# Optimization experiments

Hardware: AMD Instinct MI355X
Metric: run time of the kernel (lower is better)

## Reference

```python
import jax, jax.numpy as jnp
import numpy as np

B, T, I, H = 64, 512, 512, 512


def setup_inputs() -> dict:
    key = jax.random.key(0)
    ks = jax.random.split(key, 7)
    xavier_std = float(np.sqrt(2.0 / (B + H)))  # matches xavier_normal_ on [B,H]
    w_scale = float(1.0 / np.sqrt(H))           # ~ pytorch LSTMCell default scale
    return {
        "x": jax.random.normal(ks[0], (B, T, I), dtype=jnp.float32),
        "h0": jax.random.normal(ks[1], (B, H), dtype=jnp.float32) * xavier_std,
        "c0": jax.random.normal(ks[2], (B, H), dtype=jnp.float32) * xavier_std,
        "W_ih": jax.random.normal(ks[3], (4 * H, I), dtype=jnp.float32) * w_scale,
        "W_hh": jax.random.normal(ks[4], (4 * H, H), dtype=jnp.float32) * w_scale,
        "b_ih": jax.random.normal(ks[5], (4 * H,), dtype=jnp.float32) * w_scale,
        "b_hh": jax.random.normal(ks[6], (4 * H,), dtype=jnp.float32) * w_scale,
    }


def lstm_forward(x, h0, c0, W_ih, W_hh, b_ih, b_hh):
    # Precompute the input-to-gate projection for all timesteps in one big GEMM.
    # xg: [T, B, 4H]
    xg = jnp.einsum("bti,gi->tbg", x, W_ih) + (b_ih + b_hh)

    def step(carry, xg_t):
        h, c = carry
        gates = xg_t + h @ W_hh.T  # [B, 4H]
        i, f, g, o = jnp.split(gates, 4, axis=-1)
        i = jax.nn.sigmoid(i)
        f = jax.nn.sigmoid(f)
        g = jnp.tanh(g)
        o = jax.nn.sigmoid(o)
        c = f * c + i * g
        h = o * jnp.tanh(c)
        return (h, c), h

    (h_T, c_T), outs = jax.lax.scan(step, (h0, c0), xg)
    output = jnp.transpose(outs, (1, 0, 2))  # [B, T, H]
    return output, h_T, c_T


def reference(x, h0, c0, W_ih, W_hh, b_ih, b_hh):
    return lstm_forward(x, h0, c0, W_ih, W_hh, b_ih, b_hh)
```

## Files before the change

kernel.cpp:

```cpp
#include <hip/hip_runtime.h>
#include <hip/hip_fp16.h>
#include <string.h>

constexpr int B = 64, T = 512, I = 512, H = 512, G = 2048;

typedef _Float16 half8 __attribute__((ext_vector_type(8)));
typedef float floatx4 __attribute__((ext_vector_type(4)));

__global__ __launch_bounds__(256, 2) void xg_gemm(
    const float* __restrict__ x,
    const float* __restrict__ W_ih,
    const float* __restrict__ b_ih,
    const float* __restrict__ b_hh,
    _Float16* __restrict__ xg)
{
    const int tid  = threadIdx.x;
    const int wave = tid >> 6, lane = tid & 63;
    const int quad = lane >> 4, col = lane & 15;
    const int rowA = blockIdx.x * 128 + wave * 16;
    const int rowB = rowA + 64;

    __shared__ __align__(16) _Float16 xs[64][264];

    half8 wfA[16], wfB[16];
    {
        const float* wpA = W_ih + (size_t)(rowA + col) * I;
        const float* wpB = W_ih + (size_t)(rowB + col) * I;
#pragma unroll
        for (int kc = 0; kc < 16; ++kc) {
            half8 vA, vB;
#pragma unroll
            for (int j = 0; j < 8; ++j) {
                vA[j] = (_Float16)wpA[kc * 32 + quad * 8 + j];
                vB[j] = (_Float16)wpB[kc * 32 + quad * 8 + j];
            }
            wfA[kc] = vA; wfB[kc] = vB;
        }
    }
    float biasA[4], biasB[4];
#pragma unroll
    for (int r = 0; r < 4; ++r) {
        biasA[r] = b_ih[rowA + quad * 4 + r] + b_hh[rowA + quad * 4 + r];
        biasB[r] = b_ih[rowB + quad * 4 + r] + b_hh[rowB + quad * 4 + r];
    }

    for (int ti = 0; ti < 4; ++ti) {
        const int t = blockIdx.y * 4 + ti;
        floatx4 accA[4], accB[4];
#pragma unroll
        for (int nt = 0; nt < 4; ++nt) {
            accA[nt] = (floatx4){0.f, 0.f, 0.f, 0.f};
            accB[nt] = (floatx4){0.f, 0.f, 0.f, 0.f};
        }

        for (int hfl = 0; hfl < 2; ++hfl) {
            __syncthreads();
#pragma unroll 4
            for (int c = 0; c < 16; ++c) {
                int idx = c * 256 + tid;
                int row = idx >> 6;
                int kk  = (idx & 63) * 4;
                const float4 v = *(const float4*)(x + ((size_t)row * T + t) * I + hfl * 256 + kk);
                xs[row][kk + 0] = (_Float16)v.x;
                xs[row][kk + 1] = (_Float16)v.y;
                xs[row][kk + 2] = (_Float16)v.z;
                xs[row][kk + 3] = (_Float16)v.w;
            }
            __syncthreads();
#pragma unroll
            for (int kc = 0; kc < 8; ++kc) {
#pragma unroll
                for (int nt = 0; nt < 4; ++nt) {
                    const half8 bfr = *(const half8*)&xs[nt * 16 + col][kc * 32 + quad * 8];
                    accA[nt] = __builtin_amdgcn_mfma_f32_16x16x32_f16(
                        wfA[hfl * 8 + kc], bfr, accA[nt], 0, 0, 0);
                    accB[nt] = __builtin_amdgcn_mfma_f32_16x16x32_f16(
                        wfB[hfl * 8 + kc], bfr, accB[nt], 0, 0, 0);
                }
            }
        }
#pragma unroll
        for (int nt = 0; nt < 4; ++nt) {
            int b = nt * 16 + col;
#pragma unroll
            for (int r = 0; r < 4; ++r) {
                xg[((size_t)t * G + rowA + quad * 4 + r) * B + b] = (_Float16)(accA[nt][r] + biasA[r]);
                xg[((size_t)t * G + rowB + quad * 4 + r) * B + b] = (_Float16)(accB[nt][r] + biasB[r]);
            }
        }
    }
}

__global__ __launch_bounds__(256, 1) void lstm_rec(
    const float* __restrict__ h0,
    const float* __restrict__ c0,
    const float* __restrict__ W_hh,
    const _Float16* __restrict__ xg,
    _Float16* __restrict__ hbuf,
    unsigned int* __restrict__ cnts,
    float* __restrict__ out)
{
    const int blk  = blockIdx.x;
    const int bg   = blk & 3;
    const int hg   = blk >> 2;
    const int tid  = threadIdx.x;
    const int wave = tid >> 6, lane = tid & 63;
    const int quad = lane >> 4, col = lane & 15;

    const int bglob = bg * 16 + col;
    const int hbase = hg * 32 + wave * 8;

    unsigned int* cnt = cnts + bg * 64;

    int arow0 = (col < 8) ? (hbase + col) : (512 + hbase + col - 8);
    int arow1 = arow0 + 1024;
    half8 wf0[16], wf1[16];
#pragma unroll
    for (int kc = 0; kc < 16; ++kc) {
        const float* p0 = W_hh + (size_t)arow0 * H + kc * 32 + quad * 8;
        const float* p1 = W_hh + (size_t)arow1 * H + kc * 32 + quad * 8;
        half8 v0, v1;
#pragma unroll
        for (int j = 0; j < 8; ++j) { v0[j] = (_Float16)p0[j]; v1[j] = (_Float16)p1[j]; }
        wf0[kc] = v0; wf1[kc] = v1;
    }

    int xrow0[4], xrow1[4];
#pragma unroll
    for (int r = 0; r < 4; ++r) {
        int lr = quad * 4 + r;
        xrow0[r] = (lr < 8) ? (hbase + lr) : (512 + hbase + lr - 8);
        xrow1[r] = xrow0[r] + 1024;
    }

    float c[4];
#pragma unroll
    for (int r = 0; r < 4; ++r)
        c[r] = c0[(size_t)bglob * H + hbase + (quad & 1) * 4 + r];

    _Float16* hb0 = hbuf + ((size_t)0 * 4 + bg) * 16 * 512;
    _Float16* hb1 = hbuf + ((size_t)1 * 4 + bg) * 16 * 512;

    if (quad < 2) {
        _Float16 v4[4];
#pragma unroll
        for (int r = 0; r < 4; ++r)
            v4[r] = (_Float16)h0[(size_t)bglob * H + hbase + (quad & 1) * 4 + r];
        unsigned long long uv; __builtin_memcpy(&uv, v4, 8);
        __hip_atomic_store((unsigned long long*)(hb0 + (size_t)col * 512 + hbase + (quad & 1) * 4),
                           uv, __ATOMIC_RELAXED, __HIP_MEMORY_SCOPE_AGENT);
    }
    asm volatile("s_waitcnt vmcnt(0)" ::: "memory");
    __syncthreads();
    if (tid == 0)
        __hip_atomic_fetch_add(cnt, 1u, __ATOMIC_RELAXED, __HIP_MEMORY_SCOPE_AGENT);

    float xp0[4], xp1[4];
#pragma unroll
    for (int r = 0; r < 4; ++r) {
        xp0[r] = (float)xg[(size_t)xrow0[r] * B + bglob];
        xp1[r] = (float)xg[(size_t)xrow1[r] * B + bglob];
    }

    while (__hip_atomic_load(cnt, __ATOMIC_RELAXED, __HIP_MEMORY_SCOPE_AGENT) < 16u) {}
    asm volatile("" ::: "memory");

    float hh[4] = {0.f, 0.f, 0.f, 0.f};

    for (int t = 0; t < T; ++t) {
        const _Float16* hcur = (t & 1) ? hb1 : hb0;
        _Float16*       hnxt = (t & 1) ? hb0 : hb1;

        unsigned long long hu0[16], hu1[16];
#pragma unroll
        for (int kc = 0; kc < 16; ++kc) {
            unsigned long long* hp =
                (unsigned long long*)(hcur + (size_t)col * 512 + kc * 32 + quad * 8);
            hu0[kc] = __hip_atomic_load(hp,     __ATOMIC_RELAXED, __HIP_MEMORY_SCOPE_AGENT);
            hu1[kc] = __hip_atomic_load(hp + 1, __ATOMIC_RELAXED, __HIP_MEMORY_SCOPE_AGENT);
        }

        floatx4 acc0 = (floatx4){0.f, 0.f, 0.f, 0.f};
        floatx4 acc1 = (floatx4){0.f, 0.f, 0.f, 0.f};
#pragma unroll
        for (int kc = 0; kc < 16; ++kc) {
            half8 bfr;
            __builtin_memcpy(&bfr, &hu0[kc], 8);
            __builtin_memcpy((char*)&bfr + 8, &hu1[kc], 8);
            acc0 = __builtin_amdgcn_mfma_f32_16x16x32_f16(wf0[kc], bfr, acc0, 0, 0, 0);
            acc1 = __builtin_amdgcn_mfma_f32_16x16x32_f16(wf1[kc], bfr, acc1, 0, 0, 0);
        }

        float p0[4], p1[4];
#pragma unroll
        for (int r = 0; r < 4; ++r) {
            p0[r] = acc0[r] + xp0[r];
            p1[r] = acc1[r] + xp1[r];
        }
        float e0[4], e1[4];
#pragma unroll
        for (int r = 0; r < 4; ++r) {
            e0[r] = __shfl_xor(p0[r], 32);
            e1[r] = __shfl_xor(p1[r], 32);
        }
#pragma unroll
        for (int r = 0; r < 4; ++r) {
            float iv = (quad < 2) ? p0[r] : e0[r];
            float fv = (quad < 2) ? e0[r] : p0[r];
            float gv = (quad < 2) ? p1[r] : e1[r];
            float ov = (quad < 2) ? e1[r] : p1[r];
            float ii = 1.f / (1.f + __expf(-iv));
            float ff = 1.f / (1.f + __expf(-fv));
            float eg = __expf(-2.f * gv);
            float gg = (1.f - eg) / (1.f + eg);
            float oo = 1.f / (1.f + __expf(-ov));
            float cn = ff * c[r] + ii * gg;
            c[r] = cn;
            float ec = __expf(-2.f * cn);
            hh[r] = oo * ((1.f - ec) / (1.f + ec));
        }
        if (quad < 2) {
            _Float16 v4[4] = {(_Float16)hh[0], (_Float16)hh[1],
                              (_Float16)hh[2], (_Float16)hh[3]};
            unsigned long long uv; __builtin_memcpy(&uv, v4, 8);
            __hip_atomic_store((unsigned long long*)(hnxt + (size_t)col * 512 + hbase + (quad & 1) * 4),
                               uv, __ATOMIC_RELAXED, __HIP_MEMORY_SCOPE_AGENT);
            float* op = out + ((size_t)bglob * T + t) * H + hbase + (quad & 1) * 4;
            op[0] = hh[0]; op[1] = hh[1]; op[2] = hh[2]; op[3] = hh[3];
        }

        asm volatile("s_waitcnt vmcnt(0)" ::: "memory");
        __syncthreads();
        if (tid == 0)
            __hip_atomic_fetch_add(cnt, 1u, __ATOMIC_RELAXED, __HIP_MEMORY_SCOPE_AGENT);

        if (t + 1 < T) {
            const _Float16* xgt = xg + (size_t)(t + 1) * G * B;
#pragma unroll
            for (int r = 0; r < 4; ++r) {
                xp0[r] = (float)xgt[(size_t)xrow0[r] * B + bglob];
                xp1[r] = (float)xgt[(size_t)xrow1[r] * B + bglob];
            }
            const unsigned int tgt = 16u * (unsigned)(t + 2);
            while (__hip_atomic_load(cnt, __ATOMIC_RELAXED, __HIP_MEMORY_SCOPE_AGENT) < tgt) {}
            asm volatile("" ::: "memory");
        }
    }

    if (quad < 2) {
        float* hT = out + (size_t)B * T * H;
        float* cT = hT + (size_t)B * H;
#pragma unroll
        for (int r = 0; r < 4; ++r) {
            int jj = (quad & 1) * 4 + r;
            hT[(size_t)bglob * H + hbase + jj] = hh[r];
            cT[(size_t)bglob * H + hbase + jj] = c[r];
        }
    }
}

extern "C" void kernel_launch(void* const* d_in, const int* in_sizes, int n_in,
                              void* d_out, int out_size, void* d_ws, size_t ws_size,
                              hipStream_t stream) {
    const float* x    = (const float*)d_in[0];
    const float* h0   = (const float*)d_in[1];
    const float* c0   = (const float*)d_in[2];
    const float* W_ih = (const float*)d_in[3];
    const float* W_hh = (const float*)d_in[4];
    const float* b_ih = (const float*)d_in[5];
    const float* b_hh = (const float*)d_in[6];
    float* out = (float*)d_out;

    unsigned int* cnts = (unsigned int*)d_ws;
    _Float16* hbuf = (_Float16*)((char*)d_ws + 2048);
    _Float16* xg   = (_Float16*)((char*)d_ws + 2048 + (size_t)2 * 4 * 16 * 512 * 2);

    hipMemsetAsync(d_ws, 0, 2048, stream);

    xg_gemm<<<dim3(16, 128), 256, 0, stream>>>(x, W_ih, b_ih, b_hh, xg);
    lstm_rec<<<64, 256, 0, stream>>>(h0, c0, W_hh, xg, hbuf, cnts, out);
}
```

Measured before the change: 3.112 ms.

## Replace block-wide atomic counter barrier with per-wave flags polled by whole wave

The cross-block step barrier changes from a __syncthreads plus a single atomic fetch_add counter to one flag per wave (64 flags per batch group). Each wave stores its own timestep flag, and every wave polls all 64 flags in parallel with one load per lane and __all. The next-step xg prefetch is moved before the MFMA loop so its latency overlaps compute, and the output store is moved after the flag publish. This removes the intra-block barrier and atomic RMW contention, at the cost of more polling traffic and a dependence on relaxed-ordering assumptions.

```diff
diff --git a/kernel.cpp b/kernel.cpp
--- a/kernel.cpp
+++ b/kernel.cpp
@@ -97,7 +97,7 @@
     const float* __restrict__ W_hh,
     const _Float16* __restrict__ xg,
     _Float16* __restrict__ hbuf,
-    unsigned int* __restrict__ cnts,
+    unsigned int* __restrict__ flags,
     float* __restrict__ out)
 {
     const int blk  = blockIdx.x;
@@ -110,7 +110,8 @@
     const int bglob = bg * 16 + col;
     const int hbase = hg * 32 + wave * 8;
 
-    unsigned int* cnt = cnts + bg * 64;
+    unsigned int* flg   = flags + bg * 64;
+    unsigned int* myflg = flg + hg * 4 + wave;
 
     int arow0 = (col < 8) ? (hbase + col) : (512 + hbase + col - 8);
     int arow1 = arow0 + 1024;
@@ -151,9 +152,8 @@
                            uv, __ATOMIC_RELAXED, __HIP_MEMORY_SCOPE_AGENT);
     }
     asm volatile("s_waitcnt vmcnt(0)" ::: "memory");
-    __syncthreads();
-    if (tid == 0)
-        __hip_atomic_fetch_add(cnt, 1u, __ATOMIC_RELAXED, __HIP_MEMORY_SCOPE_AGENT);
+    if (lane == 0)
+        __hip_atomic_store(myflg, 1u, __ATOMIC_RELAXED, __HIP_MEMORY_SCOPE_AGENT);
 
     float xp0[4], xp1[4];
 #pragma unroll
@@ -162,7 +162,10 @@
         xp1[r] = (float)xg[(size_t)xrow1[r] * B + bglob];
     }
 
-    while (__hip_atomic_load(cnt, __ATOMIC_RELAXED, __HIP_MEMORY_SCOPE_AGENT) < 16u) {}
+    for (;;) {
+        unsigned f = __hip_atomic_load(flg + lane, __ATOMIC_RELAXED, __HIP_MEMORY_SCOPE_AGENT);
+        if (__all(f >= 1u)) break;
+    }
     asm volatile("" ::: "memory");
 
     float hh[4] = {0.f, 0.f, 0.f, 0.f};
@@ -178,6 +181,17 @@
                 (unsigned long long*)(hcur + (size_t)col * 512 + kc * 32 + quad * 8);
             hu0[kc] = __hip_atomic_load(hp,     __ATOMIC_RELAXED, __HIP_MEMORY_SCOPE_AGENT);
             hu1[kc] = __hip_atomic_load(hp + 1, __ATOMIC_RELAXED, __HIP_MEMORY_SCOPE_AGENT);
+        }
+        asm volatile("" ::: "memory");
+
+        float xn0[4], xn1[4];
+        if (t + 1 < T) {
+            const _Float16* xgt = xg + (size_t)(t + 1) * G * B;
+#pragma unroll
+            for (int r = 0; r < 4; ++r) {
+                xn0[r] = (float)xgt[(size_t)xrow0[r] * B + bglob];
+                xn1[r] = (float)xgt[(size_t)xrow1[r] * B + bglob];
+            }
         }
 
         floatx4 acc0 = (floatx4){0.f, 0.f, 0.f, 0.f};
@@ -225,24 +239,25 @@
             unsigned long long uv; __builtin_memcpy(&uv, v4, 8);
             __hip_atomic_store((unsigned long long*)(hnxt + (size_t)col * 512 + hbase + (quad & 1) * 4),
                                uv, __ATOMIC_RELAXED, __HIP_MEMORY_SCOPE_AGENT);
+        }
+
+        asm volatile("s_waitcnt vmcnt(0)" ::: "memory");
+        if (lane == 0)
+            __hip_atomic_store(myflg, (unsigned)(t + 2), __ATOMIC_RELAXED, __HIP_MEMORY_SCOPE_AGENT);
+
+        if (quad < 2) {
             float* op = out + ((size_t)bglob * T + t) * H + hbase + (quad & 1) * 4;
             op[0] = hh[0]; op[1] = hh[1]; op[2] = hh[2]; op[3] = hh[3];
         }
 
-        asm volatile("s_waitcnt vmcnt(0)" ::: "memory");
-        __syncthreads();
-        if (tid == 0)
-            __hip_atomic_fetch_add(cnt, 1u, __ATOMIC_RELAXED, __HIP_MEMORY_SCOPE_AGENT);
-
         if (t + 1 < T) {
-            const _Float16* xgt = xg + (size_t)(t + 1) * G * B;
-#pragma unroll
-            for (int r = 0; r < 4; ++r) {
-                xp0[r] = (float)xgt[(size_t)xrow0[r] * B + bglob];
-                xp1[r] = (float)xgt[(size_t)xrow1[r] * B + bglob];
-            }
-            const unsigned int tgt = 16u * (unsigned)(t + 2);
-            while (__hip_atomic_load(cnt, __ATOMIC_RELAXED, __HIP_MEMORY_SCOPE_AGENT) < tgt) {}
+#pragma unroll
+            for (int r = 0; r < 4; ++r) { xp0[r] = xn0[r]; xp1[r] = xn1[r]; }
+            const unsigned tgt = (unsigned)(t + 2);
+            for (;;) {
+                unsigned f = __hip_atomic_load(flg + lane, __ATOMIC_RELAXED, __HIP_MEMORY_SCOPE_AGENT);
+                if (__all(f >= tgt)) break;
+            }
             asm volatile("" ::: "memory");
         }
     }
@@ -271,12 +286,12 @@
     const float* b_hh = (const float*)d_in[6];
     float* out = (float*)d_out;
 
-    unsigned int* cnts = (unsigned int*)d_ws;
+    unsigned int* flags = (unsigned int*)d_ws;
     _Float16* hbuf = (_Float16*)((char*)d_ws + 2048);
     _Float16* xg   = (_Float16*)((char*)d_ws + 2048 + (size_t)2 * 4 * 16 * 512 * 2);
 
     hipMemsetAsync(d_ws, 0, 2048, stream);
 
     xg_gemm<<<dim3(16, 128), 256, 0, stream>>>(x, W_ih, b_ih, b_hh, xg);
-    lstm_rec<<<64, 256, 0, stream>>>(h0, c0, W_hh, xg, hbuf, cnts, out);
+    lstm_rec<<<64, 256, 0, stream>>>(h0, c0, W_hh, xg, hbuf, flags, out);
 }
```

Result: slower. 4.528 ms (+45.5%).
